# Kernel tuning notes

Hardware: AMD Instinct MI355X
Metric: run time of the kernel (lower is better)

The kernel has to match this reference:

```python
import jax, jax.numpy as jnp
import numpy as np

MODES1 = 16
MODES2 = 16
WIDTH = 64


def spectral_conv2d(x, w):
    # x: [b, ci, n1, n2] real; w: [ci, co, m1, m2, 2] real (re, im)
    b, ci, n1, n2 = x.shape
    co, m1, m2 = w.shape[1], w.shape[2], w.shape[3]
    x_ft = jnp.fft.rfft2(x, norm='ortho')              # [b, ci, n1, n2//2+1] complex
    wc = w[..., 0] + 1j * w[..., 1]                     # [ci, co, m1, m2]
    blk = jnp.einsum('bixy,ioxy->boxy', x_ft[:, :, :m1, :m2], wc)
    out_ft = jnp.zeros((b, co, n1, n2 // 2 + 1), dtype=x_ft.dtype)
    out_ft = out_ft.at[:, :, :m1, :m2].set(blk)
    return jnp.fft.irfft2(out_ft, s=(n1, n2), norm='ortho')


def conv1x1(x, w, bias):
    # x: [b, ci, n1, n2]; w: [co, ci]; bias: [co]
    return jnp.einsum('bixy,oi->boxy', x, w) + bias[None, :, None, None]


def setup_inputs() -> dict:
    key = jax.random.key(0)
    ks = jax.random.split(key, 20)
    B, CIN, N1, N2 = 16, 3, 256, 256
    W = WIDTH
    scale = 1.0 / (W * W)
    inp = {
        'x': jax.random.normal(ks[0], (B, CIN, N1, N2), dtype=jnp.float32),
        'fc0_w': jax.random.normal(ks[1], (W, CIN), dtype=jnp.float32) * 0.1,
        'fc0_b': jnp.zeros((W,), dtype=jnp.float32),
        'sw1': scale * jax.random.normal(ks[2], (W, W, MODES1, MODES2, 2), dtype=jnp.float32),
        'sw2': scale * jax.random.normal(ks[3], (W, W, MODES1, MODES2, 2), dtype=jnp.float32),
        'sw3': scale * jax.random.normal(ks[4], (W, W, MODES1, MODES2, 2), dtype=jnp.float32),
        'sw4': scale * jax.random.normal(ks[5], (W, W, MODES1, MODES2, 2), dtype=jnp.float32),
        'cw1': jax.random.normal(ks[6], (W, W), dtype=jnp.float32) * 0.05,
        'cb1': jnp.zeros((W,), dtype=jnp.float32),
        'cw2': jax.random.normal(ks[7], (W, W), dtype=jnp.float32) * 0.05,
        'cb2': jnp.zeros((W,), dtype=jnp.float32),
        'cw3': jax.random.normal(ks[8], (W, W), dtype=jnp.float32) * 0.05,
        'cb3': jnp.zeros((W,), dtype=jnp.float32),
        'cw4': jax.random.normal(ks[9], (W, W), dtype=jnp.float32) * 0.05,
        'cb4': jnp.zeros((W,), dtype=jnp.float32),
        'fc1_w': jax.random.normal(ks[10], (64, W), dtype=jnp.float32) * 0.05,
        'fc1_b': jnp.zeros((64,), dtype=jnp.float32),
        'fc2_w': jax.random.normal(ks[11], (1, 64), dtype=jnp.float32) * 0.05,
        'fc2_b': jnp.zeros((1,), dtype=jnp.float32),
    }
    return inp


def reference(x, fc0_w, fc0_b, sw1, sw2, sw3, sw4,
              cw1, cb1, cw2, cb2, cw3, cb3, cw4, cb4,
              fc1_w, fc1_b, fc2_w, fc2_b):
    # lift: [b, c, n1, n2] -> channels-last Linear -> [b, width, n1, n2]
    h = jnp.einsum('bcxy,wc->bwxy', x, fc0_w) + fc0_b[None, :, None, None]
    for sw, cw, cb in ((sw1, cw1, cb1), (sw2, cw2, cb2), (sw3, cw3, cb3), (sw4, cw4, cb4)):
        h = jax.nn.gelu(spectral_conv2d(h, sw) + conv1x1(h, cw, cb), approximate=False)
    # projection head (channels-last linears)
    h = jax.nn.gelu(jnp.einsum('bwxy,fw->bfxy', h, fc1_w) + fc1_b[None, :, None, None], approximate=False)
    out = jnp.einsum('bfxy,of->boxy', h, fc2_w) + fc2_b[None, :, None, None]
    return out
```

## Files before the change

kernel.cpp:

```cpp
#include <hip/hip_runtime.h>
#include <math.h>


typedef unsigned int   u32;
typedef unsigned short u16;
typedef __attribute__((ext_vector_type(8))) __bf16 bf16x8;
typedef __attribute__((ext_vector_type(4))) float  f32x4;

constexpr long F1_B  = 134217728;
constexpr long G_B   = 150994944;
constexpr long F2_B  = 167772160;
constexpr long CC_B  = 169869312;
constexpr long WF_B  = 171966464;
constexpr long WXI_B = 171999232;
constexpr long TWF_B = 172032000;
constexpr long BAS_B = 172048384;

__device__ __forceinline__ float gelu_exact(float v) {
    return 0.5f * v * (1.0f + erff(v * 0.70710678118654752440f));
}
__device__ __forceinline__ float bflo(u32 u) { return __uint_as_float(u << 16); }
__device__ __forceinline__ float bfhi(u32 u) { return __uint_as_float(u & 0xffff0000u); }
__device__ __forceinline__ u16 f2bf(float f) {
    u32 u = __float_as_uint(f);
    u += 0x7fffu + ((u >> 16) & 1u);
    return (u16)(u >> 16);
}
__device__ __forceinline__ u32 pack2bf(float a, float b) {
    return (u32)f2bf(a) | ((u32)f2bf(b) << 16);
}

__global__ __launch_bounds__(256) void k_tab(float* __restrict__ wf,
                                             float* __restrict__ wxi,
                                             u16* __restrict__ twf,
                                             u16* __restrict__ bas) {
    const int t = blockIdx.x * 256 + threadIdx.x;
    if (t < 4096) {
        const int y = t >> 4, k = t & 15;
        const int m = (k * y) & 255;
        double s, c; sincospi((double)m / 128.0, &s, &c);
        wf[t * 2] = (float)c; wf[t * 2 + 1] = (float)(-s);
    } else if (t < 8192) {
        const int u = t - 4096;
        const int k1 = u >> 8, x = u & 255;
        const int m = (k1 * x) & 255;
        double s, c; sincospi((double)m / 128.0, &s, &c);
        wxi[u * 2] = (float)c; wxi[u * 2 + 1] = (float)s;
    } else if (t < 16384) {
        const int u = t - 8192;
        const int kc = u >> 8, y = u & 255;
        const int k2 = kc >> 1;
        const int m = (k2 * y) & 255;
        double s, c; sincospi((double)m / 128.0, &s, &c);
        twf[kc * 256 + y] = f2bf((kc & 1) ? (float)(-s) : (float)c);
    } else {
        const int u = t - 16384;
        const int y = u >> 5, kc = u & 31;
        const int k2 = kc >> 1;
        const int m = (k2 * y) & 255;
        double s, c; sincospi((double)m / 128.0, &s, &c);
        const float cc = (k2 == 0) ? 1.0f : 2.0f;
        bas[y * 32 + kc] = f2bf((kc & 1) ? (float)(-cc * s) : (float)(cc * c));
    }
}

__device__ __forceinline__ void f1_epilogue(const u16* HO, const u16* __restrict__ twf,
                                            u16* __restrict__ f1, int b, int x, int tid) {
    const int lane = tid & 63, wave = tid >> 6;
    const int quad = lane >> 4, col = lane & 15;
    f32x4 acc0 = {0.f, 0.f, 0.f, 0.f}, acc1 = {0.f, 0.f, 0.f, 0.f};
    const int m = wave * 16 + col;
    #pragma unroll
    for (int ks = 0; ks < 8; ks++) {
        bf16x8 af = *(const bf16x8*)(HO + m * 264 + ks * 32 + quad * 8);
        bf16x8 b0 = *(const bf16x8*)(twf + col * 256 + ks * 32 + quad * 8);
        bf16x8 b1 = *(const bf16x8*)(twf + (16 + col) * 256 + ks * 32 + quad * 8);
        acc0 = __builtin_amdgcn_mfma_f32_16x16x32_bf16(af, b0, acc0, 0, 0, 0);
        acc1 = __builtin_amdgcn_mfma_f32_16x16x32_bf16(af, b1, acc1, 0, 0, 0);
    }
    #pragma unroll
    for (int r = 0; r < 4; r++) {
        const int o = wave * 16 + quad * 4 + r;
        u16* dst = f1 + (((long)(b * 64 + o)) * 256 + x) * 32;
        dst[col]      = f2bf(acc0[r]);
        dst[16 + col] = f2bf(acc1[r]);
    }
}

__global__ __launch_bounds__(256) void k_lift(const float* __restrict__ xin,
                                              const float* __restrict__ w0,
                                              const float* __restrict__ b0,
                                              u16* __restrict__ h,
                                              const u16* __restrict__ twf,
                                              u16* __restrict__ f1) {
    __shared__ float ws0[192];
    __shared__ float bs0[64];
    __shared__ u16 HO[64 * 264];
    const int tid = threadIdx.x;
    if (tid < 192) ws0[tid] = w0[tid];
    if (tid < 64)  bs0[tid] = b0[tid];
    __syncthreads();
    const int b = blockIdx.x >> 8, x = blockIdx.x & 255;
    const long pix = (((long)b * 3) * 256 + x) * 256 + tid;
    const float x0 = xin[pix];
    const float x1 = xin[pix + 65536];
    const float x2 = xin[pix + 131072];
    u16* hp = h + ((long)b * 64) * 65536 + x * 256 + tid;
    #pragma unroll 4
    for (int w = 0; w < 64; w++) {
        float v = bs0[w];
        v = fmaf(x0, ws0[w * 3],     v);
        v = fmaf(x1, ws0[w * 3 + 1], v);
        v = fmaf(x2, ws0[w * 3 + 2], v);
        const u16 bf = f2bf(v);
        hp[(long)w * 65536] = bf;
        HO[w * 264 + tid] = bf;
    }
    __syncthreads();
    f1_epilogue(HO, twf, f1, b, x, tid);
}

__global__ __launch_bounds__(256) void k_dftx(const u16* __restrict__ f1,
                                              const float* __restrict__ wf,
                                              float* __restrict__ f2) {
    const int tid = threadIdx.x;
    const int k1 = tid >> 4, k2 = tid & 15;
    const u16* base = f1 + (long)blockIdx.x * 8192;
    float cr0 = 0, ci0 = 0, cr1 = 0, ci1 = 0;
    for (int x = 0; x < 256; x += 2) {
        const u32 wa = *(const u32*)(base + x * 32 + k2 * 2);
        const float2 ta = *(const float2*)(wf + x * 32 + k1 * 2);
        const float Far = bflo(wa), Fai = bfhi(wa);
        cr0 = fmaf(Far, ta.x, fmaf(-Fai, ta.y, cr0));
        ci0 = fmaf(Fai, ta.x, fmaf(Far, ta.y, ci0));
        const u32 wb = *(const u32*)(base + (x + 1) * 32 + k2 * 2);
        const float2 tb = *(const float2*)(wf + (x + 1) * 32 + k1 * 2);
        const float Fbr = bflo(wb), Fbi = bfhi(wb);
        cr1 = fmaf(Fbr, tb.x, fmaf(-Fbi, tb.y, cr1));
        ci1 = fmaf(Fbi, tb.x, fmaf(Fbr, tb.y, ci1));
    }
    const int m = k1 * 16 + k2;
    *(float2*)(f2 + ((long)m * 1024 + blockIdx.x) * 2) =
        make_float2(cr0 + cr1, ci0 + ci1);
}

__global__ __launch_bounds__(256) void k_mode(const float* __restrict__ f2,
                                              const float* __restrict__ sw,
                                              float* __restrict__ cc) {
    __shared__ __align__(16) float wsh[8192];
    __shared__ __align__(16) float fsh[2048];
    const int tid = threadIdx.x;
    const int m = blockIdx.x;
    const float scale = 1.0f / 65536.0f;
    for (int p = tid; p < 4096; p += 256) {
        const float2 w = *(const float2*)(sw + ((long)p * 256 + m) * 2);
        wsh[p * 2]     = w.x * scale;
        wsh[p * 2 + 1] = w.y * scale;
    }
    for (int t = tid; t < 2048; t += 256) fsh[t] = f2[(long)m * 2048 + t];
    __syncthreads();
    const int b = tid >> 4, o0 = (tid & 15) * 4;
    float re[4] = {0, 0, 0, 0}, im[4] = {0, 0, 0, 0};
    for (int i = 0; i < 64; i++) {
        const float2 F = *(const float2*)(fsh + (b * 64 + i) * 2);
        #pragma unroll
        for (int oo = 0; oo < 4; oo++) {
            const float2 W = *(const float2*)(wsh + (i * 64 + o0 + oo) * 2);
            re[oo] = fmaf(F.x, W.x, fmaf(-F.y, W.y, re[oo]));
            im[oo] = fmaf(F.x, W.y, fmaf(F.y, W.x, im[oo]));
        }
    }
    #pragma unroll
    for (int oo = 0; oo < 4; oo++) {
        *(float2*)(cc + ((long)m * 1024 + b * 64 + o0 + oo) * 2) =
            make_float2(re[oo], im[oo]);
    }
}

__global__ __launch_bounds__(256) void k_invx(const float* __restrict__ cc,
                                              const float* __restrict__ wxi,
                                              u16* __restrict__ g) {
    __shared__ __align__(16) float csh[512];
    const int tid = threadIdx.x;
    const int blk = blockIdx.x;
    ((float2*)csh)[tid] = *(const float2*)(cc + ((long)tid * 1024 + blk) * 2);
    __syncthreads();
    const int x = tid;
    float ar[16], ai[16];
    #pragma unroll
    for (int k = 0; k < 16; k++) { ar[k] = 0; ai[k] = 0; }
    for (int k1 = 0; k1 < 16; k1++) {
        const float2 t = *(const float2*)(wxi + (k1 * 256 + x) * 2);
        #pragma unroll
        for (int k2 = 0; k2 < 16; k2++) {
            const float2 C = ((const float2*)csh)[k1 * 16 + k2];
            ar[k2] = fmaf(C.x, t.x, fmaf(-C.y, t.y, ar[k2]));
            ai[k2] = fmaf(C.x, t.y, fmaf(C.y, t.x, ai[k2]));
        }
    }
    u32 wbuf[16];
    #pragma unroll
    for (int k = 0; k < 16; k++) wbuf[k] = pack2bf(ar[k], ai[k]);
    u16* ob = g + ((long)blk * 256 + x) * 32;
    #pragma unroll
    for (int q = 0; q < 4; q++) *(uint4*)(ob + q * 8) = ((uint4*)wbuf)[q];
}

__device__ __forceinline__ void conv_phase1(
    const u16* __restrict__ h, const u16* __restrict__ Gbf,
    const float* __restrict__ cw, const float* __restrict__ cb,
    const u16* __restrict__ bas,
    u16* AB, u16* HO, float* cbs,
    long hbase, int b, int x, int tid, f32x4 (*acc)[4])
{
    for (int p = tid; p < 4096; p += 256) {
        const float f = cw[p];
        const u16 hi = f2bf(f);
        const u16 lo = f2bf(f - __uint_as_float((u32)hi << 16));
        AB[(p >> 6) * 168 + (p & 63)]      = hi;
        AB[(p >> 6) * 168 + 64 + (p & 63)] = lo;
    }
    {
        const int o = tid >> 2, cg = tid & 3;
        const uint4 q = *(const uint4*)(Gbf + (((long)(b * 64 + o)) * 256 + x) * 32 + cg * 8);
        *(uint4*)(AB + o * 168 + 128 + cg * 8) = q;
    }
    if (tid < 64) cbs[tid] = cb[tid];
    {
        const int i = tid & 63, yc = tid >> 6;
        const u16* hs = h + hbase + (long)i * 65536 + yc * 64;
        u16* d = HO + i;
        #pragma unroll
        for (int u = 0; u < 8; u++) {
            const uint4 q = *(const uint4*)(hs + u * 8);
            const int y0 = yc * 64 + u * 8;
            d[(y0 + 0) * 72] = (u16)q.x;  d[(y0 + 1) * 72] = (u16)(q.x >> 16);
            d[(y0 + 2) * 72] = (u16)q.y;  d[(y0 + 3) * 72] = (u16)(q.y >> 16);
            d[(y0 + 4) * 72] = (u16)q.z;  d[(y0 + 5) * 72] = (u16)(q.z >> 16);
            d[(y0 + 6) * 72] = (u16)q.w;  d[(y0 + 7) * 72] = (u16)(q.w >> 16);
        }
    }
    __syncthreads();
    const int lane = tid & 63, wave = tid >> 6;
    const int quad = lane >> 4, col = lane & 15;
    const int ybase = wave * 64;
    #pragma unroll
    for (int ks = 0; ks < 5; ks++) {
        bf16x8 bfr[4];
        if (ks < 4) {
            const int krow = (ks & 1) * 32 + quad * 8;
            #pragma unroll
            for (int nt = 0; nt < 4; nt++)
                bfr[nt] = *(const bf16x8*)(HO + (ybase + nt * 16 + col) * 72 + krow);
        } else {
            #pragma unroll
            for (int nt = 0; nt < 4; nt++)
                bfr[nt] = *(const bf16x8*)(bas + (ybase + nt * 16 + col) * 32 + quad * 8);
        }
        #pragma unroll
        for (int mt = 0; mt < 4; mt++) {
            const bf16x8 af = *(const bf16x8*)(AB + (mt * 16 + col) * 168 + ks * 32 + quad * 8);
            #pragma unroll
            for (int nt = 0; nt < 4; nt++)
                acc[mt][nt] = __builtin_amdgcn_mfma_f32_16x16x32_bf16(af, bfr[nt], acc[mt][nt], 0, 0, 0);
        }
    }
    __syncthreads();
}

__global__ __launch_bounds__(256) void k_conv(u16* __restrict__ h,
                                              const u16* __restrict__ Gbf,
                                              const float* __restrict__ cw,
                                              const float* __restrict__ cb,
                                              const u16* __restrict__ bas,
                                              const u16* __restrict__ twf,
                                              u16* __restrict__ f1) {
    __shared__ u16 AB[64 * 168];
    __shared__ u16 HO[18432];
    __shared__ float cbs[64];
    const int tid = threadIdx.x;
    const int b = blockIdx.x >> 8, x = blockIdx.x & 255;
    const long hbase = (long)b * 4194304 + x * 256;
    f32x4 acc[4][4];
    const f32x4 z = {0.f, 0.f, 0.f, 0.f};
    #pragma unroll
    for (int i = 0; i < 4; i++)
        #pragma unroll
        for (int j = 0; j < 4; j++) acc[i][j] = z;
    conv_phase1(h, Gbf, cw, cb, bas, AB, HO, cbs, hbase, b, x, tid, acc);
    const int lane = tid & 63, wave = tid >> 6;
    const int quad = lane >> 4, col = lane & 15;
    const int ybase = wave * 64;
    #pragma unroll
    for (int mt = 0; mt < 4; mt++)
        #pragma unroll
        for (int nt = 0; nt < 4; nt++)
            #pragma unroll
            for (int r = 0; r < 4; r++) {
                const int o = mt * 16 + quad * 4 + r;
                const int y = ybase + nt * 16 + col;
                HO[o * 264 + y] = f2bf(gelu_exact(acc[mt][nt][r] + cbs[o]));
            }
    __syncthreads();
    {
        const int o = tid >> 2, cg = tid & 3;
        u16* dh = h + hbase + (long)o * 65536 + cg * 64;
        const u16* so = HO + o * 264 + cg * 64;
        #pragma unroll
        for (int u = 0; u < 8; u++)
            *(uint4*)(dh + u * 8) = *(const uint4*)(so + u * 8);
    }
    f1_epilogue(HO, twf, f1, b, x, tid);
}

__global__ __launch_bounds__(256) void k_conv_head(const u16* __restrict__ h,
                                                   const u16* __restrict__ Gbf,
                                                   const float* __restrict__ cw,
                                                   const float* __restrict__ cb,
                                                   const u16* __restrict__ bas,
                                                   const float* __restrict__ w1,
                                                   const float* __restrict__ b1,
                                                   const float* __restrict__ w2,
                                                   const float* __restrict__ b2,
                                                   float* __restrict__ out) {
    __shared__ u16 AB[64 * 168];
    __shared__ u16 HO[18432];
    __shared__ float cbs[64];
    __shared__ float b1s[64], w2s[64];
    const int tid = threadIdx.x;
    const int b = blockIdx.x >> 8, x = blockIdx.x & 255;
    const long hbase = (long)b * 4194304 + x * 256;
    const float bias2 = b2[0];
    f32x4 acc[4][4];
    const f32x4 z = {0.f, 0.f, 0.f, 0.f};
    #pragma unroll
    for (int i = 0; i < 4; i++)
        #pragma unroll
        for (int j = 0; j < 4; j++) acc[i][j] = z;
    conv_phase1(h, Gbf, cw, cb, bas, AB, HO, cbs, hbase, b, x, tid, acc);
    const int lane = tid & 63, wave = tid >> 6;
    const int quad = lane >> 4, col = lane & 15;
    const int ybase = wave * 64;
    #pragma unroll
    for (int mt = 0; mt < 4; mt++)
        #pragma unroll
        for (int nt = 0; nt < 4; nt++)
            #pragma unroll
            for (int r = 0; r < 4; r++) {
                const int o = mt * 16 + quad * 4 + r;
                const int y = ybase + nt * 16 + col;
                HO[y * 72 + o] = f2bf(gelu_exact(acc[mt][nt][r] + cbs[o]));
            }
    for (int p = tid; p < 4096; p += 256) {
        const float f = w1[p];
        const u16 hi = f2bf(f);
        const u16 lo = f2bf(f - __uint_as_float((u32)hi << 16));
        AB[(p >> 6) * 168 + (p & 63)]      = hi;
        AB[(p >> 6) * 168 + 64 + (p & 63)] = lo;
    }
    if (tid < 64) { b1s[tid] = b1[tid]; w2s[tid] = w2[tid]; }
    __syncthreads();
    f32x4 acc2[4][4];
    #pragma unroll
    for (int i = 0; i < 4; i++)
        #pragma unroll
        for (int j = 0; j < 4; j++) acc2[i][j] = z;
    #pragma unroll
    for (int ks = 0; ks < 4; ks++) {
        const int krow = (ks & 1) * 32 + quad * 8;
        bf16x8 bfr[4];
        #pragma unroll
        for (int nt = 0; nt < 4; nt++)
            bfr[nt] = *(const bf16x8*)(HO + (ybase + nt * 16 + col) * 72 + krow);
        #pragma unroll
        for (int mt = 0; mt < 4; mt++) {
            const bf16x8 af = *(const bf16x8*)(AB + (mt * 16 + col) * 168 + ks * 32 + quad * 8);
            #pragma unroll
            for (int nt = 0; nt < 4; nt++)
                acc2[mt][nt] = __builtin_amdgcn_mfma_f32_16x16x32_bf16(af, bfr[nt], acc2[mt][nt], 0, 0, 0);
        }
    }
    float p4[4] = {0.f, 0.f, 0.f, 0.f};
    #pragma unroll
    for (int mt = 0; mt < 4; mt++)
        #pragma unroll
        for (int r = 0; r < 4; r++) {
            const int f = mt * 16 + quad * 4 + r;
            const float bb = b1s[f], ww = w2s[f];
            #pragma unroll
            for (int nt = 0; nt < 4; nt++)
                p4[nt] = fmaf(ww, gelu_exact(acc2[mt][nt][r] + bb), p4[nt]);
        }
    #pragma unroll
    for (int nt = 0; nt < 4; nt++) {
        p4[nt] += __shfl_xor(p4[nt], 16);
        p4[nt] += __shfl_xor(p4[nt], 32);
    }
    out[(long)b * 65536 + x * 256 + ybase + lane] = p4[quad] + bias2;
}

extern "C" void kernel_launch(void* const* d_in, const int* in_sizes, int n_in,
                              void* d_out, int out_size, void* d_ws, size_t ws_size,
                              hipStream_t stream) {
    const float* x     = (const float*)d_in[0];
    const float* fc0_w = (const float*)d_in[1];
    const float* fc0_b = (const float*)d_in[2];
    const float* sw[4] = {(const float*)d_in[3], (const float*)d_in[4],
                          (const float*)d_in[5], (const float*)d_in[6]};
    const float* cwA[4] = {(const float*)d_in[7],  (const float*)d_in[9],
                           (const float*)d_in[11], (const float*)d_in[13]};
    const float* cbA[4] = {(const float*)d_in[8],  (const float*)d_in[10],
                           (const float*)d_in[12], (const float*)d_in[14]};
    const float* fc1_w = (const float*)d_in[15];
    const float* fc1_b = (const float*)d_in[16];
    const float* fc2_w = (const float*)d_in[17];
    const float* fc2_b = (const float*)d_in[18];

    char* base = (char*)d_ws;
    u16*   h    = (u16*)base;
    u16*   f1   = (u16*)(base + F1_B);
    u16*   Gbf  = (u16*)(base + G_B);
    float* f2   = (float*)(base + F2_B);
    float* cbuf = (float*)(base + CC_B);
    float* wf   = (float*)(base + WF_B);
    float* wxi  = (float*)(base + WXI_B);
    u16*   twf  = (u16*)(base + TWF_B);
    u16*   bas  = (u16*)(base + BAS_B);

    k_tab<<<96, 256, 0, stream>>>(wf, wxi, twf, bas);
    k_lift<<<4096, 256, 0, stream>>>(x, fc0_w, fc0_b, h, twf, f1);
    for (int l = 0; l < 4; l++) {
        k_dftx<<<1024, 256, 0, stream>>>(f1, wf, f2);
        k_mode<<<256, 256, 0, stream>>>(f2, sw[l], cbuf);
        k_invx<<<1024, 256, 0, stream>>>(cbuf, wxi, Gbf);
        if (l < 3) {
            k_conv<<<4096, 256, 0, stream>>>(h, Gbf, cwA[l], cbA[l], bas, twf, f1);
        } else {
            k_conv_head<<<4096, 256, 0, stream>>>(h, Gbf, cwA[3], cbA[3], bas,
                                                  fc1_w, fc1_b, fc2_w, fc2_b,
                                                  (float*)d_out);
        }
    }
}
```

Baseline: 1.092 ms.

## Store activations channels-last and pre-split conv weights once into bf16 hi/lo

Switches the activation buffer h from channel-planar to pixel-major channels-last layout. The conv kernels can then load MFMA B fragments straight from global memory instead of transposing h through LDS. The fp32-to-bf16 hi/lo split of the 1x1 conv and fc1 weights moves into a one-time k_wsplit kernel, which removes per-block weight conversion and the AB shared buffer. Epilogues write packed vectors, and the f1 DFT epilogue now reads a transposed LDS tile with strided scalar gathers. Occupancy is hinted with launch_bounds(256,3), at the cost of possible bank conflicts in the gathered LDS reads.

```diff
diff --git a/kernel.cpp b/kernel.cpp
--- a/kernel.cpp
+++ b/kernel.cpp
@@ -15,6 +15,11 @@
 constexpr long WXI_B = 171999232;
 constexpr long TWF_B = 172032000;
 constexpr long BAS_B = 172048384;
+constexpr long WSP_B = 172064768;
+
+constexpr int HOP = 76;
+
+union BU { uint2 u2[2]; uint4 u4; bf16x8 v; u16 s[8]; };
 
 __device__ __forceinline__ float gelu_exact(float v) {
     return 0.5f * v * (1.0f + erff(v * 0.70710678118654752440f));
@@ -64,27 +69,49 @@
     }
 }
 
-__device__ __forceinline__ void f1_epilogue(const u16* HO, const u16* __restrict__ twf,
-                                            u16* __restrict__ f1, int b, int x, int tid) {
+__global__ __launch_bounds__(256) void k_wsplit(const float* __restrict__ c1,
+                                                const float* __restrict__ c2,
+                                                const float* __restrict__ c3,
+                                                const float* __restrict__ c4,
+                                                const float* __restrict__ f1w,
+                                                u16* __restrict__ wsp) {
+    const int t = blockIdx.x * 256 + threadIdx.x;
+    const int w = t >> 12, p = t & 4095;
+    const float* src = (w == 0) ? c1 : (w == 1) ? c2 : (w == 2) ? c3
+                     : (w == 3) ? c4 : f1w;
+    const float f = src[p];
+    const u16 hi = f2bf(f);
+    const u16 lo = f2bf(f - __uint_as_float((u32)hi << 16));
+    u16* dst = wsp + w * 8192 + (p >> 6) * 128 + (p & 63);
+    dst[0]  = hi;
+    dst[64] = lo;
+}
+
+__device__ __forceinline__ void f1t_epilogue(const u16* HOyo,
+                                             const u16* __restrict__ twf,
+                                             u16* __restrict__ f1,
+                                             int b, int x, int tid) {
     const int lane = tid & 63, wave = tid >> 6;
     const int quad = lane >> 4, col = lane & 15;
-    f32x4 acc0 = {0.f, 0.f, 0.f, 0.f}, acc1 = {0.f, 0.f, 0.f, 0.f};
-    const int m = wave * 16 + col;
+    const int o = wave * 16 + col;
+    f32x4 a0 = {0.f, 0.f, 0.f, 0.f}, a1 = {0.f, 0.f, 0.f, 0.f};
     #pragma unroll
     for (int ks = 0; ks < 8; ks++) {
-        bf16x8 af = *(const bf16x8*)(HO + m * 264 + ks * 32 + quad * 8);
-        bf16x8 b0 = *(const bf16x8*)(twf + col * 256 + ks * 32 + quad * 8);
-        bf16x8 b1 = *(const bf16x8*)(twf + (16 + col) * 256 + ks * 32 + quad * 8);
-        acc0 = __builtin_amdgcn_mfma_f32_16x16x32_bf16(af, b0, acc0, 0, 0, 0);
-        acc1 = __builtin_amdgcn_mfma_f32_16x16x32_bf16(af, b1, acc1, 0, 0, 0);
-    }
-    #pragma unroll
-    for (int r = 0; r < 4; r++) {
-        const int o = wave * 16 + quad * 4 + r;
-        u16* dst = f1 + (((long)(b * 64 + o)) * 256 + x) * 32;
-        dst[col]      = f2bf(acc0[r]);
-        dst[16 + col] = f2bf(acc1[r]);
-    }
+        const int kb = ks * 32 + quad * 8;
+        BU bb;
+        #pragma unroll
+        for (int j = 0; j < 8; j++) bb.s[j] = HOyo[(kb + j) * HOP + o];
+        const bf16x8 af0 = *(const bf16x8*)(twf + col * 256 + kb);
+        const bf16x8 af1 = *(const bf16x8*)(twf + (16 + col) * 256 + kb);
+        a0 = __builtin_amdgcn_mfma_f32_16x16x32_bf16(af0, bb.v, a0, 0, 0, 0);
+        a1 = __builtin_amdgcn_mfma_f32_16x16x32_bf16(af1, bb.v, a1, 0, 0, 0);
+    }
+    u16* dst = f1 + (((long)(b * 64 + o)) * 256 + x) * 32 + quad * 4;
+    uint2 w;
+    w.x = pack2bf(a0[0], a0[1]); w.y = pack2bf(a0[2], a0[3]);
+    *(uint2*)dst = w;
+    w.x = pack2bf(a1[0], a1[1]); w.y = pack2bf(a1[2], a1[3]);
+    *(uint2*)(dst + 16) = w;
 }
 
 __global__ __launch_bounds__(256) void k_lift(const float* __restrict__ xin,
@@ -93,9 +120,8 @@
                                               u16* __restrict__ h,
                                               const u16* __restrict__ twf,
                                               u16* __restrict__ f1) {
-    __shared__ float ws0[192];
-    __shared__ float bs0[64];
-    __shared__ u16 HO[64 * 264];
+    __shared__ float ws0[192], bs0[64];
+    __shared__ u16 HOyo[256 * HOP];
     const int tid = threadIdx.x;
     if (tid < 192) ws0[tid] = w0[tid];
     if (tid < 64)  bs0[tid] = b0[tid];
@@ -105,19 +131,23 @@
     const float x0 = xin[pix];
     const float x1 = xin[pix + 65536];
     const float x2 = xin[pix + 131072];
-    u16* hp = h + ((long)b * 64) * 65536 + x * 256 + tid;
-    #pragma unroll 4
-    for (int w = 0; w < 64; w++) {
-        float v = bs0[w];
-        v = fmaf(x0, ws0[w * 3],     v);
-        v = fmaf(x1, ws0[w * 3 + 1], v);
-        v = fmaf(x2, ws0[w * 3 + 2], v);
-        const u16 bf = f2bf(v);
-        hp[(long)w * 65536] = bf;
-        HO[w * 264 + tid] = bf;
-    }
-    __syncthreads();
-    f1_epilogue(HO, twf, f1, b, x, tid);
+    u32 pr[32];
+    #pragma unroll
+    for (int w = 0; w < 64; w += 2) {
+        float v0 = bs0[w], v1 = bs0[w + 1];
+        v0 = fmaf(x0, ws0[w * 3],     v0);  v1 = fmaf(x0, ws0[w * 3 + 3], v1);
+        v0 = fmaf(x1, ws0[w * 3 + 1], v0);  v1 = fmaf(x1, ws0[w * 3 + 4], v1);
+        v0 = fmaf(x2, ws0[w * 3 + 2], v0);  v1 = fmaf(x2, ws0[w * 3 + 5], v1);
+        pr[w >> 1] = pack2bf(v0, v1);
+    }
+    u16* hrow = h + (((long)(b * 256 + x)) << 14) + (long)tid * 64;
+    #pragma unroll
+    for (int q = 0; q < 8; q++) *(uint4*)(hrow + q * 8) = ((uint4*)pr)[q];
+    #pragma unroll
+    for (int q = 0; q < 16; q++)
+        *(uint2*)(HOyo + tid * HOP + q * 4) = ((uint2*)pr)[q];
+    __syncthreads();
+    f1t_epilogue(HOyo, twf, f1, b, x, tid);
 }
 
 __global__ __launch_bounds__(256) void k_dftx(const u16* __restrict__ f1,
@@ -206,130 +236,109 @@
     for (int q = 0; q < 4; q++) *(uint4*)(ob + q * 8) = ((uint4*)wbuf)[q];
 }
 
-__device__ __forceinline__ void conv_phase1(
-    const u16* __restrict__ h, const u16* __restrict__ Gbf,
-    const float* __restrict__ cw, const float* __restrict__ cb,
-    const u16* __restrict__ bas,
-    u16* AB, u16* HO, float* cbs,
-    long hbase, int b, int x, int tid, f32x4 (*acc)[4])
-{
-    for (int p = tid; p < 4096; p += 256) {
-        const float f = cw[p];
-        const u16 hi = f2bf(f);
-        const u16 lo = f2bf(f - __uint_as_float((u32)hi << 16));
-        AB[(p >> 6) * 168 + (p & 63)]      = hi;
-        AB[(p >> 6) * 168 + 64 + (p & 63)] = lo;
-    }
-    {
-        const int o = tid >> 2, cg = tid & 3;
-        const uint4 q = *(const uint4*)(Gbf + (((long)(b * 64 + o)) * 256 + x) * 32 + cg * 8);
-        *(uint4*)(AB + o * 168 + 128 + cg * 8) = q;
-    }
-    if (tid < 64) cbs[tid] = cb[tid];
-    {
-        const int i = tid & 63, yc = tid >> 6;
-        const u16* hs = h + hbase + (long)i * 65536 + yc * 64;
-        u16* d = HO + i;
-        #pragma unroll
-        for (int u = 0; u < 8; u++) {
-            const uint4 q = *(const uint4*)(hs + u * 8);
-            const int y0 = yc * 64 + u * 8;
-            d[(y0 + 0) * 72] = (u16)q.x;  d[(y0 + 1) * 72] = (u16)(q.x >> 16);
-            d[(y0 + 2) * 72] = (u16)q.y;  d[(y0 + 3) * 72] = (u16)(q.y >> 16);
-            d[(y0 + 4) * 72] = (u16)q.z;  d[(y0 + 5) * 72] = (u16)(q.z >> 16);
-            d[(y0 + 6) * 72] = (u16)q.w;  d[(y0 + 7) * 72] = (u16)(q.w >> 16);
-        }
-    }
-    __syncthreads();
+__device__ __forceinline__ void conv_phase1(const u16* __restrict__ h, long hbase,
+                                            const u16* __restrict__ Gbf,
+                                            const u16* __restrict__ wsp,
+                                            const u16* __restrict__ bas,
+                                            int b, int x, int tid, f32x4 (*acc)[4]) {
     const int lane = tid & 63, wave = tid >> 6;
     const int quad = lane >> 4, col = lane & 15;
-    const int ybase = wave * 64;
-    #pragma unroll
-    for (int ks = 0; ks < 5; ks++) {
-        bf16x8 bfr[4];
-        if (ks < 4) {
-            const int krow = (ks & 1) * 32 + quad * 8;
+    #pragma unroll
+    for (int ks = 0; ks < 2; ks++) {
+        bf16x8 B[4], Ah[4], Al[4];
+        #pragma unroll
+        for (int nt = 0; nt < 4; nt++) {
+            const int y = wave * 64 + nt * 16 + col;
+            B[nt] = *(const bf16x8*)(h + hbase + (long)y * 64 + ks * 32 + quad * 8);
+        }
+        #pragma unroll
+        for (int mt = 0; mt < 4; mt++) {
+            Ah[mt] = *(const bf16x8*)(wsp + (mt * 16 + col) * 128 + ks * 32 + quad * 8);
+            Al[mt] = *(const bf16x8*)(wsp + (mt * 16 + col) * 128 + 64 + ks * 32 + quad * 8);
+        }
+        #pragma unroll
+        for (int mt = 0; mt < 4; mt++)
+            #pragma unroll
+            for (int nt = 0; nt < 4; nt++) {
+                acc[mt][nt] = __builtin_amdgcn_mfma_f32_16x16x32_bf16(Ah[mt], B[nt], acc[mt][nt], 0, 0, 0);
+                acc[mt][nt] = __builtin_amdgcn_mfma_f32_16x16x32_bf16(Al[mt], B[nt], acc[mt][nt], 0, 0, 0);
+            }
+    }
+    {
+        bf16x8 B[4], Ag[4];
+        #pragma unroll
+        for (int nt = 0; nt < 4; nt++) {
+            const int y = wave * 64 + nt * 16 + col;
+            B[nt] = *(const bf16x8*)(bas + y * 32 + quad * 8);
+        }
+        #pragma unroll
+        for (int mt = 0; mt < 4; mt++)
+            Ag[mt] = *(const bf16x8*)(Gbf + (((long)(b * 64 + mt * 16 + col)) * 256 + x) * 32 + quad * 8);
+        #pragma unroll
+        for (int mt = 0; mt < 4; mt++)
             #pragma unroll
             for (int nt = 0; nt < 4; nt++)
-                bfr[nt] = *(const bf16x8*)(HO + (ybase + nt * 16 + col) * 72 + krow);
-        } else {
-            #pragma unroll
-            for (int nt = 0; nt < 4; nt++)
-                bfr[nt] = *(const bf16x8*)(bas + (ybase + nt * 16 + col) * 32 + quad * 8);
-        }
-        #pragma unroll
-        for (int mt = 0; mt < 4; mt++) {
-            const bf16x8 af = *(const bf16x8*)(AB + (mt * 16 + col) * 168 + ks * 32 + quad * 8);
-            #pragma unroll
-            for (int nt = 0; nt < 4; nt++)
-                acc[mt][nt] = __builtin_amdgcn_mfma_f32_16x16x32_bf16(af, bfr[nt], acc[mt][nt], 0, 0, 0);
-        }
-    }
-    __syncthreads();
-}
-
-__global__ __launch_bounds__(256) void k_conv(u16* __restrict__ h,
-                                              const u16* __restrict__ Gbf,
-                                              const float* __restrict__ cw,
-                                              const float* __restrict__ cb,
-                                              const u16* __restrict__ bas,
-                                              const u16* __restrict__ twf,
-                                              u16* __restrict__ f1) {
-    __shared__ u16 AB[64 * 168];
-    __shared__ u16 HO[18432];
+                acc[mt][nt] = __builtin_amdgcn_mfma_f32_16x16x32_bf16(Ag[mt], B[nt], acc[mt][nt], 0, 0, 0);
+    }
+}
+
+__global__ __launch_bounds__(256, 3) void k_conv(u16* __restrict__ h,
+                                                 const u16* __restrict__ Gbf,
+                                                 const u16* __restrict__ wsp,
+                                                 const float* __restrict__ cb,
+                                                 const u16* __restrict__ bas,
+                                                 const u16* __restrict__ twf,
+                                                 u16* __restrict__ f1) {
+    __shared__ u16 HOyo[256 * HOP];
     __shared__ float cbs[64];
     const int tid = threadIdx.x;
     const int b = blockIdx.x >> 8, x = blockIdx.x & 255;
-    const long hbase = (long)b * 4194304 + x * 256;
+    const long hbase = ((long)(b * 256 + x)) << 14;
+    if (tid < 64) cbs[tid] = cb[tid];
     f32x4 acc[4][4];
     const f32x4 z = {0.f, 0.f, 0.f, 0.f};
     #pragma unroll
     for (int i = 0; i < 4; i++)
         #pragma unroll
         for (int j = 0; j < 4; j++) acc[i][j] = z;
-    conv_phase1(h, Gbf, cw, cb, bas, AB, HO, cbs, hbase, b, x, tid, acc);
+    conv_phase1(h, hbase, Gbf, wsp, bas, b, x, tid, acc);
+    __syncthreads();
     const int lane = tid & 63, wave = tid >> 6;
     const int quad = lane >> 4, col = lane & 15;
-    const int ybase = wave * 64;
-    #pragma unroll
-    for (int mt = 0; mt < 4; mt++)
-        #pragma unroll
-        for (int nt = 0; nt < 4; nt++)
-            #pragma unroll
-            for (int r = 0; r < 4; r++) {
-                const int o = mt * 16 + quad * 4 + r;
-                const int y = ybase + nt * 16 + col;
-                HO[o * 264 + y] = f2bf(gelu_exact(acc[mt][nt][r] + cbs[o]));
-            }
-    __syncthreads();
-    {
-        const int o = tid >> 2, cg = tid & 3;
-        u16* dh = h + hbase + (long)o * 65536 + cg * 64;
-        const u16* so = HO + o * 264 + cg * 64;
-        #pragma unroll
-        for (int u = 0; u < 8; u++)
-            *(uint4*)(dh + u * 8) = *(const uint4*)(so + u * 8);
-    }
-    f1_epilogue(HO, twf, f1, b, x, tid);
-}
-
-__global__ __launch_bounds__(256) void k_conv_head(const u16* __restrict__ h,
-                                                   const u16* __restrict__ Gbf,
-                                                   const float* __restrict__ cw,
-                                                   const float* __restrict__ cb,
-                                                   const u16* __restrict__ bas,
-                                                   const float* __restrict__ w1,
-                                                   const float* __restrict__ b1,
-                                                   const float* __restrict__ w2,
-                                                   const float* __restrict__ b2,
-                                                   float* __restrict__ out) {
-    __shared__ u16 AB[64 * 168];
-    __shared__ u16 HO[18432];
-    __shared__ float cbs[64];
-    __shared__ float b1s[64], w2s[64];
+    #pragma unroll
+    for (int mt = 0; mt < 4; mt++) {
+        const int o0 = mt * 16 + quad * 4;
+        const float c0 = cbs[o0], c1 = cbs[o0 + 1], c2 = cbs[o0 + 2], c3 = cbs[o0 + 3];
+        #pragma unroll
+        for (int nt = 0; nt < 4; nt++) {
+            const int y = wave * 64 + nt * 16 + col;
+            uint2 w;
+            w.x = pack2bf(gelu_exact(acc[mt][nt][0] + c0), gelu_exact(acc[mt][nt][1] + c1));
+            w.y = pack2bf(gelu_exact(acc[mt][nt][2] + c2), gelu_exact(acc[mt][nt][3] + c3));
+            *(uint2*)(h + hbase + (long)y * 64 + o0) = w;
+            *(uint2*)(HOyo + y * HOP + o0) = w;
+        }
+    }
+    __syncthreads();
+    f1t_epilogue(HOyo, twf, f1, b, x, tid);
+}
+
+__global__ __launch_bounds__(256, 3) void k_conv_head(const u16* __restrict__ h,
+                                                      const u16* __restrict__ Gbf,
+                                                      const u16* __restrict__ wsp,
+                                                      const float* __restrict__ cb,
+                                                      const u16* __restrict__ bas,
+                                                      const u16* __restrict__ w1sp,
+                                                      const float* __restrict__ b1,
+                                                      const float* __restrict__ w2,
+                                                      const float* __restrict__ b2,
+                                                      float* __restrict__ out) {
+    __shared__ u16 HOyo[256 * HOP];
+    __shared__ float cbs[64], b1s[64], w2s[64];
     const int tid = threadIdx.x;
     const int b = blockIdx.x >> 8, x = blockIdx.x & 255;
-    const long hbase = (long)b * 4194304 + x * 256;
+    const long hbase = ((long)(b * 256 + x)) << 14;
+    if (tid < 64) { cbs[tid] = cb[tid]; b1s[tid] = b1[tid]; w2s[tid] = w2[tid]; }
     const float bias2 = b2[0];
     f32x4 acc[4][4];
     const f32x4 z = {0.f, 0.f, 0.f, 0.f};
@@ -337,28 +346,23 @@
     for (int i = 0; i < 4; i++)
         #pragma unroll
         for (int j = 0; j < 4; j++) acc[i][j] = z;
-    conv_phase1(h, Gbf, cw, cb, bas, AB, HO, cbs, hbase, b, x, tid, acc);
+    conv_phase1(h, hbase, Gbf, wsp, bas, b, x, tid, acc);
+    __syncthreads();
     const int lane = tid & 63, wave = tid >> 6;
     const int quad = lane >> 4, col = lane & 15;
-    const int ybase = wave * 64;
-    #pragma unroll
-    for (int mt = 0; mt < 4; mt++)
-        #pragma unroll
-        for (int nt = 0; nt < 4; nt++)
-            #pragma unroll
-            for (int r = 0; r < 4; r++) {
-                const int o = mt * 16 + quad * 4 + r;
-                const int y = ybase + nt * 16 + col;
-                HO[y * 72 + o] = f2bf(gelu_exact(acc[mt][nt][r] + cbs[o]));
-            }
-    for (int p = tid; p < 4096; p += 256) {
-        const float f = w1[p];
-        const u16 hi = f2bf(f);
-        const u16 lo = f2bf(f - __uint_as_float((u32)hi << 16));
-        AB[(p >> 6) * 168 + (p & 63)]      = hi;
-        AB[(p >> 6) * 168 + 64 + (p & 63)] = lo;
-    }
-    if (tid < 64) { b1s[tid] = b1[tid]; w2s[tid] = w2[tid]; }
+    #pragma unroll
+    for (int mt = 0; mt < 4; mt++) {
+        const int o0 = mt * 16 + quad * 4;
+        const float c0 = cbs[o0], c1 = cbs[o0 + 1], c2 = cbs[o0 + 2], c3 = cbs[o0 + 3];
+        #pragma unroll
+        for (int nt = 0; nt < 4; nt++) {
+            const int y = wave * 64 + nt * 16 + col;
+            uint2 w;
+            w.x = pack2bf(gelu_exact(acc[mt][nt][0] + c0), gelu_exact(acc[mt][nt][1] + c1));
+            w.y = pack2bf(gelu_exact(acc[mt][nt][2] + c2), gelu_exact(acc[mt][nt][3] + c3));
+            *(uint2*)(HOyo + y * HOP + o0) = w;
+        }
+    }
     __syncthreads();
     f32x4 acc2[4][4];
     #pragma unroll
@@ -367,18 +371,24 @@
         for (int j = 0; j < 4; j++) acc2[i][j] = z;
     #pragma unroll
     for (int ks = 0; ks < 4; ks++) {
-        const int krow = (ks & 1) * 32 + quad * 8;
-        bf16x8 bfr[4];
-        #pragma unroll
-        for (int nt = 0; nt < 4; nt++)
-            bfr[nt] = *(const bf16x8*)(HO + (ybase + nt * 16 + col) * 72 + krow);
-        #pragma unroll
-        for (int mt = 0; mt < 4; mt++) {
-            const bf16x8 af = *(const bf16x8*)(AB + (mt * 16 + col) * 168 + ks * 32 + quad * 8);
+        const int kk = (ks & 1) * 32 + quad * 8;
+        bf16x8 B[4], A[4];
+        #pragma unroll
+        for (int nt = 0; nt < 4; nt++) {
+            const int y = wave * 64 + nt * 16 + col;
+            BU bb;
+            bb.u2[0] = *(const uint2*)(HOyo + y * HOP + kk);
+            bb.u2[1] = *(const uint2*)(HOyo + y * HOP + kk + 4);
+            B[nt] = bb.v;
+        }
+        #pragma unroll
+        for (int mt = 0; mt < 4; mt++)
+            A[mt] = *(const bf16x8*)(w1sp + (mt * 16 + col) * 128 + ks * 32 + quad * 8);
+        #pragma unroll
+        for (int mt = 0; mt < 4; mt++)
             #pragma unroll
             for (int nt = 0; nt < 4; nt++)
-                acc2[mt][nt] = __builtin_amdgcn_mfma_f32_16x16x32_bf16(af, bfr[nt], acc2[mt][nt], 0, 0, 0);
-        }
+                acc2[mt][nt] = __builtin_amdgcn_mfma_f32_16x16x32_bf16(A[mt], B[nt], acc2[mt][nt], 0, 0, 0);
     }
     float p4[4] = {0.f, 0.f, 0.f, 0.f};
     #pragma unroll
@@ -396,7 +406,7 @@
         p4[nt] += __shfl_xor(p4[nt], 16);
         p4[nt] += __shfl_xor(p4[nt], 32);
     }
-    out[(long)b * 65536 + x * 256 + ybase + lane] = p4[quad] + bias2;
+    out[(long)b * 65536 + x * 256 + wave * 64 + lane] = p4[quad] + bias2;
 }
 
 extern "C" void kernel_launch(void* const* d_in, const int* in_sizes, int n_in,
@@ -426,19 +436,22 @@
     float* wxi  = (float*)(base + WXI_B);
     u16*   twf  = (u16*)(base + TWF_B);
     u16*   bas  = (u16*)(base + BAS_B);
+    u16*   wsp  = (u16*)(base + WSP_B);
 
     k_tab<<<96, 256, 0, stream>>>(wf, wxi, twf, bas);
+    k_wsplit<<<80, 256, 0, stream>>>(cwA[0], cwA[1], cwA[2], cwA[3], fc1_w, wsp);
     k_lift<<<4096, 256, 0, stream>>>(x, fc0_w, fc0_b, h, twf, f1);
     for (int l = 0; l < 4; l++) {
         k_dftx<<<1024, 256, 0, stream>>>(f1, wf, f2);
         k_mode<<<256, 256, 0, stream>>>(f2, sw[l], cbuf);
         k_invx<<<1024, 256, 0, stream>>>(cbuf, wxi, Gbf);
         if (l < 3) {
-            k_conv<<<4096, 256, 0, stream>>>(h, Gbf, cwA[l], cbA[l], bas, twf, f1);
+            k_conv<<<4096, 256, 0, stream>>>(h, Gbf, wsp + l * 8192, cbA[l],
+                                             bas, twf, f1);
         } else {
-            k_conv_head<<<4096, 256, 0, stream>>>(h, Gbf, cwA[3], cbA[3], bas,
-                                                  fc1_w, fc1_b, fc2_w, fc2_b,
-                                                  (float*)d_out);
-        }
-    }
-}
+            k_conv_head<<<4096, 256, 0, stream>>>(h, Gbf, wsp + 3 * 8192, cbA[3],
+                                                  bas, wsp + 4 * 8192, fc1_b,
+                                                  fc2_w, fc2_b, (float*)d_out);
+        }
+    }
+}
```

Result: faster. 984.9 us (-9.8%).
